# Performance work log

Hardware: AMD Instinct MI355X
Metric: run time of the kernel (lower is better)

The kernel has to match this reference:

```python
import jax, jax.numpy as jnp
import numpy as np

DELTA_V = 0.5
DELTA_D = 1.5
ALPHA = 1.0
BETA = 1.0
GAMMA = 0.001
IGNORE_LABEL = -1
MAX_VIEWS = 100
NUM_CLASSES = 19

B, D, H, W = 8, 128, 256, 256


def setup_inputs() -> dict:
    key = jax.random.key(0)
    k1, k2 = jax.random.split(key)
    feats = jax.random.normal(k1, (B, D, H, W), dtype=jnp.float32)
    labels = jax.random.randint(k2, (B, H, W), 0, NUM_CLASSES, dtype=jnp.int32)
    return {"feats": feats, "labels": labels}


def _safe_norm(sq):
    # gradient-safe sqrt: subgradient 0 at 0 (matches torch.norm at 0)
    pos = sq > 0
    return jnp.where(pos, jnp.sqrt(jnp.where(pos, sq, 1.0)), 0.0)


def reference(feats, labels):
    # feats: (B, D, H, W) -> (N, D); labels: (B, H, W) -> (N,)
    # (labels already at feats' HxW, so the nearest interpolation is identity)
    d = feats.shape[1]
    f = jnp.transpose(feats, (0, 2, 3, 1)).reshape(-1, d)
    lab = labels.reshape(-1)

    valid_pix = lab != IGNORE_LABEL
    lab0 = jnp.where(valid_pix, lab, 0)

    # per-class counts and means (vectorized replacement of the per-class loop)
    cnt = jax.ops.segment_sum(valid_pix.astype(f.dtype), lab0, num_segments=NUM_CLASSES)
    sums = jax.ops.segment_sum(jnp.where(valid_pix[:, None], f, 0.0), lab0, num_segments=NUM_CLASSES)
    safe_cnt = jnp.maximum(cnt, 1.0)
    means = sums / safe_cnt[:, None]  # (C, D)

    # class selection: present, != ignore, count > max_views
    valid_cls = cnt > MAX_VIEWS

    # --- loss_var: per-class mean of hinged distances to class mean ---
    diff = f - means[lab0]
    dist = _safe_norm(jnp.sum(diff * diff, axis=1)) - DELTA_V
    h = jnp.maximum(dist, 0.0)
    contrib = jnp.where(valid_pix & valid_cls[lab0], h * h, 0.0)
    var_c = jax.ops.segment_sum(contrib, lab0, num_segments=NUM_CLASSES) / safe_cnt
    loss_var = jnp.sum(jnp.where(valid_cls, var_c, 0.0))

    # --- loss_reg: sum of norms of class means ---
    mean_norm = _safe_norm(jnp.sum(means * means, axis=1))
    loss_reg = jnp.sum(jnp.where(valid_cls, mean_norm, 0.0))

    # --- loss_dist: faithful to the original (buggy) double loop:
    # a ranges over all T valid classes (sorted by id); b ranges over the first
    # T-1 valid classes of cluster_mean_lst, including b == a.
    cls_ids = jnp.arange(NUM_CLASSES)
    last_valid = jnp.max(jnp.where(valid_cls, cls_ids, -1))
    bmask = valid_cls & (cls_ids != last_valid)
    pd = means[:, None, :] - means[None, :, :]  # (C, C, D) -- C is tiny
    pdn = _safe_norm(jnp.sum(pd * pd, axis=-1))
    hd = jnp.maximum(2.0 * DELTA_D - pdn, 0.0)
    mask2 = valid_cls[:, None] & bmask[None, :]
    loss_dist = jnp.sum(jnp.where(mask2, hd * hd, 0.0))

    t = jnp.sum(valid_cls).astype(f.dtype)
    loss = (ALPHA * loss_var / t
            + BETA * loss_dist / (t * (t - 1.0))
            + GAMMA * loss_reg / t)
    return loss
```

## Files before the change

kernel.cpp:

```cpp
#include <hip/hip_runtime.h>

#define C 19
#define DCH 128
#define HWSZ 65536
#define TPB 256

#define WS_SUMS  0
#define WS_CNT   2432
#define WS_VAR   2451
#define WS_MEANS 2560
#define WS_VALID 4992
#define WS_SCAL  5011
#define WS_ZERO_END 2470

__global__ void k0_init(float* __restrict__ ws) {
    int i = blockIdx.x * blockDim.x + threadIdx.x;
    if (i < WS_ZERO_END) ws[i] = 0.f;
}

#define K1_NB  2048
#define K1_RPX 4096

__global__ __launch_bounds__(TPB) void k1_sums(const float* __restrict__ feats,
                                               const int* __restrict__ labels,
                                               float* __restrict__ ws) {
    __shared__ int llab[K1_RPX];

    const int t = threadIdx.x;
    const int lane = t & 63;
    const int w = t >> 6;
    const int bid = blockIdx.x;
    const int b  = bid >> 8;
    const int r  = (bid >> 4) & 15;
    const int dg = bid & 15;

    const int* lb = labels + b * HWSZ + r * K1_RPX;
    int4 myl[4];
#pragma unroll
    for (int u = 0; u < 4; ++u) {
        int4 v = *reinterpret_cast<const int4*>(lb + (u * TPB + t) * 4);
        myl[u] = v;
        *reinterpret_cast<int4*>(&llab[(u * TPB + t) * 4]) = v;
    }
    __syncthreads();

    if (dg == 0) {
        float cr[C];
#pragma unroll
        for (int c = 0; c < C; ++c) cr[c] = 0.f;
#pragma unroll
        for (int u = 0; u < 4; ++u) {
#pragma unroll
            for (int c = 0; c < C; ++c) {
                cr[c] += (myl[u].x == c ? 1.f : 0.f);
                cr[c] += (myl[u].y == c ? 1.f : 0.f);
                cr[c] += (myl[u].z == c ? 1.f : 0.f);
                cr[c] += (myl[u].w == c ? 1.f : 0.f);
            }
        }
#pragma unroll
        for (int c = 0; c < C; ++c)
            for (int m = 1; m < 64; m <<= 1) cr[c] += __shfl_xor(cr[c], m);
        float v = cr[0];
#pragma unroll
        for (int c = 1; c < C; ++c) v = (lane == c) ? cr[c] : v;
        if (lane < C) atomicAdd(&ws[WS_CNT + lane], v);
    }

#pragma unroll
    for (int dd = 0; dd < 2; ++dd) {
        const int d = dg * 8 + dd * 4 + w;
        const float* fp = feats + (((size_t)(b * DCH + d)) << 16) + r * K1_RPX;
        float acc[C];
#pragma unroll
        for (int c = 0; c < C; ++c) acc[c] = 0.f;

        for (int jb = 0; jb < 16; jb += 4) {
            float4 x[4]; int4 l[4];
#pragma unroll
            for (int u = 0; u < 4; ++u) {
                x[u] = *reinterpret_cast<const float4*>(fp + (jb + u) * 256 + lane * 4);
                l[u] = *reinterpret_cast<const int4*>(&llab[((jb + u) * 64 + lane) * 4]);
            }
#pragma unroll
            for (int u = 0; u < 4; ++u) {
#pragma unroll
                for (int c = 0; c < C; ++c) {
                    acc[c] += (l[u].x == c ? x[u].x : 0.f);
                    acc[c] += (l[u].y == c ? x[u].y : 0.f);
                    acc[c] += (l[u].z == c ? x[u].z : 0.f);
                    acc[c] += (l[u].w == c ? x[u].w : 0.f);
                }
            }
        }
#pragma unroll
        for (int c = 0; c < C; ++c)
            for (int m = 1; m < 64; m <<= 1) acc[c] += __shfl_xor(acc[c], m);
        float v = acc[0];
#pragma unroll
        for (int c = 1; c < C; ++c) v = (lane == c) ? acc[c] : v;
        if (lane < C) atomicAdd(&ws[WS_SUMS + d * C + lane], v);
    }
}

__global__ __launch_bounds__(TPB) void k2_means(float* __restrict__ ws) {
    __shared__ float lm[DCH * C];
    __shared__ float lcnt[C];
    __shared__ float lvalid[C];
    __shared__ float lreg;
    __shared__ float ldist;
    __shared__ int   llast;
    __shared__ float ltv;
    int t = threadIdx.x;
    if (t == 0) { lreg = 0.f; ldist = 0.f; }
    if (t < C) {
        float c = ws[WS_CNT + t];
        lcnt[t] = c;
        lvalid[t] = (c > 100.f) ? 1.f : 0.f;
    }
    __syncthreads();
    for (int i = t; i < DCH * C; i += TPB) {
        int c = i % C;
        float m = ws[WS_SUMS + i] / fmaxf(lcnt[c], 1.f);
        lm[i] = m;
        ws[WS_MEANS + i] = m;
    }
    if (t == 0) {
        float tv = 0.f; int last = -1;
        for (int c2 = 0; c2 < C; ++c2) if (lvalid[c2] > 0.5f) { tv += 1.f; last = c2; }
        ltv = tv; llast = last;
    }
    __syncthreads();
    if (t < C) {
        float s = 0.f;
        for (int d = 0; d < DCH; ++d) { float m = lm[d * C + t]; s += m * m; }
        float nrm = (s > 0.f) ? sqrtf(s) : 0.f;
        if (lvalid[t] > 0.5f) atomicAdd(&lreg, nrm);
    }
    for (int pr = t; pr < C * C; pr += TPB) {
        int a = pr / C, b2 = pr % C;
        if (lvalid[a] > 0.5f && lvalid[b2] > 0.5f && b2 != llast) {
            float s = 0.f;
            for (int d = 0; d < DCH; ++d) {
                float df = lm[d * C + a] - lm[d * C + b2];
                s += df * df;
            }
            float nrm = (s > 0.f) ? sqrtf(s) : 0.f;
            float hd = fmaxf(3.0f - nrm, 0.f);
            atomicAdd(&ldist, hd * hd);
        }
    }
    __syncthreads();
    if (t < C) ws[WS_VALID + t] = lvalid[t];
    if (t == 0) {
        ws[WS_SCAL + 0] = lreg;
        ws[WS_SCAL + 1] = ldist;
        ws[WS_SCAL + 2] = ltv;
    }
}

#define K3_NB 2048
#define MPAD 20

__global__ __launch_bounds__(TPB) void k3_var(const float* __restrict__ feats,
                                              const int* __restrict__ labels,
                                              float* __restrict__ ws) {
    __shared__ float lmS[DCH * MPAD];
    __shared__ float lvalid[C];
    __shared__ float lvar[C];
    const int t = threadIdx.x;
    for (int i = t; i < DCH * C; i += TPB) {
        int d = i / C, c = i - d * C;
        lmS[d * MPAD + c] = ws[WS_MEANS + i];
    }
    if (t < C) { lvalid[t] = ws[WS_VALID + t]; lvar[t] = 0.f; }
    __syncthreads();

    const int qloc = t >> 2;
    const int k = t & 3;
    const int q = blockIdx.x * 64 + qloc;
    const int b = q >> 14;
    const int p = (q & 16383) * 4;

    const int4 lab4 = *reinterpret_cast<const int4*>(labels + b * HWSZ + p);
    const int l0 = lab4.x < 0 ? 0 : lab4.x;
    const int l1 = lab4.y < 0 ? 0 : lab4.y;
    const int l2 = lab4.z < 0 ? 0 : lab4.z;
    const int l3 = lab4.w < 0 ? 0 : lab4.w;

    const float* fb = feats + (((size_t)(b * DCH + k * 32)) << 16) + p;
    float a0 = 0.f, a1 = 0.f, a2 = 0.f, a3 = 0.f;
    for (int i = 0; i < 32; i += 8) {
        float4 xb[8];
#pragma unroll
        for (int u = 0; u < 8; ++u)
            xb[u] = *reinterpret_cast<const float4*>(fb + ((size_t)(i + u) << 16));
#pragma unroll
        for (int u = 0; u < 8; ++u) {
            const float* mr = &lmS[(k * 32 + i + u) * MPAD];
            float d0 = xb[u].x - mr[l0]; a0 = fmaf(d0, d0, a0);
            float d1 = xb[u].y - mr[l1]; a1 = fmaf(d1, d1, a1);
            float d2 = xb[u].z - mr[l2]; a2 = fmaf(d2, d2, a2);
            float d3 = xb[u].w - mr[l3]; a3 = fmaf(d3, d3, a3);
        }
    }
    a0 += __shfl_xor(a0, 1); a0 += __shfl_xor(a0, 2);
    a1 += __shfl_xor(a1, 1); a1 += __shfl_xor(a1, 2);
    a2 += __shfl_xor(a2, 1); a2 += __shfl_xor(a2, 2);
    a3 += __shfl_xor(a3, 1); a3 += __shfl_xor(a3, 2);

    if (k == 0) {
        auto hinge2 = [&](float a, int rawlab, int l) -> float {
            float nrm = (a > 0.f) ? sqrtf(a) : 0.f;
            float h = fmaxf(nrm - 0.5f, 0.f);
            float v = h * h;
            return (rawlab >= 0 && lvalid[l] > 0.5f) ? v : 0.f;
        };
        atomicAdd(&lvar[l0], hinge2(a0, lab4.x, l0));
        atomicAdd(&lvar[l1], hinge2(a1, lab4.y, l1));
        atomicAdd(&lvar[l2], hinge2(a2, lab4.z, l2));
        atomicAdd(&lvar[l3], hinge2(a3, lab4.w, l3));
    }
    __syncthreads();
    if (t < C) atomicAdd(&ws[WS_VAR + t], lvar[t]);
}

__global__ void k4_final(const float* __restrict__ ws, float* __restrict__ out) {
    if (threadIdx.x == 0) {
        float loss_var = 0.f;
        for (int c = 0; c < C; ++c) {
            float cnt = ws[WS_CNT + c];
            float v = ws[WS_VAR + c] / fmaxf(cnt, 1.f);
            if (ws[WS_VALID + c] > 0.5f) loss_var += v;
        }
        float reg  = ws[WS_SCAL + 0];
        float dist = ws[WS_SCAL + 1];
        float tv   = ws[WS_SCAL + 2];
        float loss = loss_var / tv + dist / (tv * (tv - 1.0f)) + 0.001f * reg / tv;
        out[0] = loss;
    }
}

extern "C" void kernel_launch(void* const* d_in, const int* in_sizes, int n_in,
                              void* d_out, int out_size, void* d_ws, size_t ws_size,
                              hipStream_t stream) {
    const float* feats  = (const float*)d_in[0];
    const int*   labels = (const int*)d_in[1];
    float* ws  = (float*)d_ws;
    float* out = (float*)d_out;

    hipLaunchKernelGGL(k0_init,  dim3((WS_ZERO_END + 255) / 256), dim3(256), 0, stream, ws);
    hipLaunchKernelGGL(k1_sums,  dim3(K1_NB), dim3(TPB), 0, stream, feats, labels, ws);
    hipLaunchKernelGGL(k2_means, dim3(1),   dim3(TPB), 0, stream, ws);
    hipLaunchKernelGGL(k3_var,   dim3(K3_NB), dim3(TPB), 0, stream, feats, labels, ws);
    hipLaunchKernelGGL(k4_final, dim3(1),   dim3(64),  0, stream, ws, out);
}
```

Before: 455.9 us.

## Compute per-class feature sums via bf16 split MFMA with one-hot label matrix

After: 491.4 us. 1.08x slower.

```diff
diff --git a/kernel.cpp b/kernel.cpp
--- a/kernel.cpp
+++ b/kernel.cpp
@@ -13,93 +13,141 @@
 #define WS_SCAL  5011
 #define WS_ZERO_END 2470
 
+typedef float f32x4 __attribute__((ext_vector_type(4)));
+typedef short bf16x8 __attribute__((ext_vector_type(8)));
+union U8 { unsigned u[4]; bf16x8 v; };
+
+__device__ inline unsigned pack_hi(float a, float b) {
+    unsigned ua = __builtin_bit_cast(unsigned, a);
+    unsigned ub = __builtin_bit_cast(unsigned, b);
+    return (ua >> 16) | (ub & 0xFFFF0000u);
+}
+__device__ inline unsigned pack_lo(float a, float b) {
+    unsigned ua = __builtin_bit_cast(unsigned, a);
+    unsigned ub = __builtin_bit_cast(unsigned, b);
+    float ra = a - __builtin_bit_cast(float, ua & 0xFFFF0000u);
+    float rb = b - __builtin_bit_cast(float, ub & 0xFFFF0000u);
+    return (__builtin_bit_cast(unsigned, ra) >> 16) |
+           (__builtin_bit_cast(unsigned, rb) & 0xFFFF0000u);
+}
+
 __global__ void k0_init(float* __restrict__ ws) {
     int i = blockIdx.x * blockDim.x + threadIdx.x;
     if (i < WS_ZERO_END) ws[i] = 0.f;
 }
 
-#define K1_NB  2048
-#define K1_RPX 4096
-
-__global__ __launch_bounds__(TPB) void k1_sums(const float* __restrict__ feats,
-                                               const int* __restrict__ labels,
-                                               float* __restrict__ ws) {
-    __shared__ int llab[K1_RPX];
+__global__ __launch_bounds__(TPB) void k1c_counts(const int* __restrict__ labels,
+                                                  float* __restrict__ ws) {
+    const int t = threadIdx.x;
+    const int lane = t & 63;
+    float cr[C];
+#pragma unroll
+    for (int c = 0; c < C; ++c) cr[c] = 0.f;
+    const int base = blockIdx.x * 8192;
+#pragma unroll
+    for (int p = 0; p < 8; ++p) {
+        int4 v = *reinterpret_cast<const int4*>(labels + base + (p * TPB + t) * 4);
+#pragma unroll
+        for (int c = 0; c < C; ++c) {
+            cr[c] += (v.x == c ? 1.f : 0.f);
+            cr[c] += (v.y == c ? 1.f : 0.f);
+            cr[c] += (v.z == c ? 1.f : 0.f);
+            cr[c] += (v.w == c ? 1.f : 0.f);
+        }
+    }
+#pragma unroll
+    for (int c = 0; c < C; ++c)
+        for (int m = 1; m < 64; m <<= 1) cr[c] += __shfl_xor(cr[c], m);
+    float v = cr[0];
+#pragma unroll
+    for (int c = 1; c < C; ++c) v = (lane == c) ? cr[c] : v;
+    if (lane < C) atomicAdd(&ws[WS_CNT + lane], v);
+}
+
+#define K1_NB  1024
+#define K1_PPB 512
+#define K1_NCH 16
+
+__global__ __launch_bounds__(TPB, 4) void k1_sums(const float* __restrict__ feats,
+                                                  const int* __restrict__ labels,
+                                                  float* __restrict__ ws) {
+    __shared__ float tileA[2][DCH * 32];
+    __shared__ int llab[K1_PPB];
 
     const int t = threadIdx.x;
     const int lane = t & 63;
     const int w = t >> 6;
-    const int bid = blockIdx.x;
-    const int b  = bid >> 8;
-    const int r  = (bid >> 4) & 15;
-    const int dg = bid & 15;
-
-    const int* lb = labels + b * HWSZ + r * K1_RPX;
-    int4 myl[4];
-#pragma unroll
-    for (int u = 0; u < 4; ++u) {
-        int4 v = *reinterpret_cast<const int4*>(lb + (u * TPB + t) * 4);
-        myl[u] = v;
-        *reinterpret_cast<int4*>(&llab[(u * TPB + t) * 4]) = v;
-    }
-    __syncthreads();
-
-    if (dg == 0) {
-        float cr[C];
-#pragma unroll
-        for (int c = 0; c < C; ++c) cr[c] = 0.f;
-#pragma unroll
-        for (int u = 0; u < 4; ++u) {
-#pragma unroll
-            for (int c = 0; c < C; ++c) {
-                cr[c] += (myl[u].x == c ? 1.f : 0.f);
-                cr[c] += (myl[u].y == c ? 1.f : 0.f);
-                cr[c] += (myl[u].z == c ? 1.f : 0.f);
-                cr[c] += (myl[u].w == c ? 1.f : 0.f);
-            }
-        }
-#pragma unroll
-        for (int c = 0; c < C; ++c)
-            for (int m = 1; m < 64; m <<= 1) cr[c] += __shfl_xor(cr[c], m);
-        float v = cr[0];
-#pragma unroll
-        for (int c = 1; c < C; ++c) v = (lane == c) ? cr[c] : v;
-        if (lane < C) atomicAdd(&ws[WS_CNT + lane], v);
-    }
-
-#pragma unroll
-    for (int dd = 0; dd < 2; ++dd) {
-        const int d = dg * 8 + dd * 4 + w;
-        const float* fp = feats + (((size_t)(b * DCH + d)) << 16) + r * K1_RPX;
-        float acc[C];
-#pragma unroll
-        for (int c = 0; c < C; ++c) acc[c] = 0.f;
-
-        for (int jb = 0; jb < 16; jb += 4) {
-            float4 x[4]; int4 l[4];
-#pragma unroll
-            for (int u = 0; u < 4; ++u) {
-                x[u] = *reinterpret_cast<const float4*>(fp + (jb + u) * 256 + lane * 4);
-                l[u] = *reinterpret_cast<const int4*>(&llab[((jb + u) * 64 + lane) * 4]);
-            }
-#pragma unroll
-            for (int u = 0; u < 4; ++u) {
-#pragma unroll
-                for (int c = 0; c < C; ++c) {
-                    acc[c] += (l[u].x == c ? x[u].x : 0.f);
-                    acc[c] += (l[u].y == c ? x[u].y : 0.f);
-                    acc[c] += (l[u].z == c ? x[u].z : 0.f);
-                    acc[c] += (l[u].w == c ? x[u].w : 0.f);
-                }
-            }
-        }
-#pragma unroll
-        for (int c = 0; c < C; ++c)
-            for (int m = 1; m < 64; m <<= 1) acc[c] += __shfl_xor(acc[c], m);
-        float v = acc[0];
-#pragma unroll
-        for (int c = 1; c < C; ++c) v = (lane == c) ? acc[c] : v;
-        if (lane < C) atomicAdd(&ws[WS_SUMS + d * C + lane], v);
+    const int b = blockIdx.x >> 7;
+    const int pbase = (blockIdx.x & 127) * K1_PPB;
+
+    if (t < K1_PPB / 4)
+        *reinterpret_cast<int4*>(&llab[t * 4]) =
+            *reinterpret_cast<const int4*>(labels + b * HWSZ + pbase + t * 4);
+
+    const int sd = t >> 3;
+    const int sg = t & 7;
+    const float* fbase = feats + (((size_t)b * DCH) << 16) + pbase;
+
+    auto stage = [&](int buf, int n) {
+#pragma unroll
+        for (int pass = 0; pass < 4; ++pass) {
+            int d = sd + pass * 32;
+            float4 x = *reinterpret_cast<const float4*>(
+                fbase + (((size_t)d) << 16) + n * 32 + sg * 4);
+            int ps = sg ^ (d & 7);
+            *reinterpret_cast<float4*>(&tileA[buf][d * 32 + ps * 4]) = x;
+        }
+    };
+
+    f32x4 acc[2][2] = {};
+    const int q8 = lane >> 4;
+    const int cc0 = lane & 15;
+    const int cc1 = 16 + cc0;
+
+    stage(0, 0);
+    for (int n = 0; n < K1_NCH; ++n) {
+        __syncthreads();
+        if (n + 1 < K1_NCH) stage((n + 1) & 1, n + 1);
+        const float* tb = tileA[n & 1];
+
+        const int* lp = &llab[n * 32 + q8 * 8];
+        int4 la = *reinterpret_cast<const int4*>(lp);
+        int4 lb = *reinterpret_cast<const int4*>(lp + 4);
+        int lv[8] = {la.x, la.y, la.z, la.w, lb.x, lb.y, lb.z, lb.w};
+        U8 B0, B1;
+#pragma unroll
+        for (int j = 0; j < 4; ++j) {
+            B0.u[j] = (lv[2*j] == cc0 ? 0x3F80u : 0u) | (lv[2*j+1] == cc0 ? 0x3F800000u : 0u);
+            B1.u[j] = (lv[2*j] == cc1 ? 0x3F80u : 0u) | (lv[2*j+1] == cc1 ? 0x3F800000u : 0u);
+        }
+
+#pragma unroll
+        for (int dt = 0; dt < 2; ++dt) {
+            int d_row = 32 * w + 16 * dt + cc0;
+            const float* rp = tb + d_row * 32;
+            int s = d_row & 7;
+            float4 xa = *reinterpret_cast<const float4*>(rp + (((2 * q8)     ^ s) * 4));
+            float4 xb = *reinterpret_cast<const float4*>(rp + (((2 * q8 + 1) ^ s) * 4));
+            U8 Ah, Al;
+            Ah.u[0] = pack_hi(xa.x, xa.y); Ah.u[1] = pack_hi(xa.z, xa.w);
+            Ah.u[2] = pack_hi(xb.x, xb.y); Ah.u[3] = pack_hi(xb.z, xb.w);
+            Al.u[0] = pack_lo(xa.x, xa.y); Al.u[1] = pack_lo(xa.z, xa.w);
+            Al.u[2] = pack_lo(xb.x, xb.y); Al.u[3] = pack_lo(xb.z, xb.w);
+            acc[dt][0] = __builtin_amdgcn_mfma_f32_16x16x32_bf16(Ah.v, B0.v, acc[dt][0], 0, 0, 0);
+            acc[dt][0] = __builtin_amdgcn_mfma_f32_16x16x32_bf16(Al.v, B0.v, acc[dt][0], 0, 0, 0);
+            acc[dt][1] = __builtin_amdgcn_mfma_f32_16x16x32_bf16(Ah.v, B1.v, acc[dt][1], 0, 0, 0);
+            acc[dt][1] = __builtin_amdgcn_mfma_f32_16x16x32_bf16(Al.v, B1.v, acc[dt][1], 0, 0, 0);
+        }
+    }
+
+#pragma unroll
+    for (int dt = 0; dt < 2; ++dt) {
+#pragma unroll
+        for (int r = 0; r < 4; ++r) {
+            int d = 32 * w + 16 * dt + q8 * 4 + r;
+            atomicAdd(&ws[WS_SUMS + d * C + cc0], acc[dt][0][r]);
+            if (cc0 < 3) atomicAdd(&ws[WS_SUMS + d * C + cc1], acc[dt][1][r]);
+        }
     }
 }
 
@@ -250,6 +298,7 @@
     float* out = (float*)d_out;
 
     hipLaunchKernelGGL(k0_init,  dim3((WS_ZERO_END + 255) / 256), dim3(256), 0, stream, ws);
+    hipLaunchKernelGGL(k1c_counts, dim3(64), dim3(TPB), 0, stream, labels, ws);
     hipLaunchKernelGGL(k1_sums,  dim3(K1_NB), dim3(TPB), 0, stream, feats, labels, ws);
     hipLaunchKernelGGL(k2_means, dim3(1),   dim3(TPB), 0, stream, ws);
     hipLaunchKernelGGL(k3_var,   dim3(K3_NB), dim3(TPB), 0, stream, feats, labels, ws);
```
